# Optimization experiments

Measured on AMD Instinct MI355X. Metric: run time of the kernel, lower is better.

## Reference

```python
import jax, jax.numpy as jnp
import numpy as np

ALPHA = 0.2  # LeakyReLU negative slope
NUM_HEADS, OUT_DIM = 8, 16
N_NODES, N_EDGES, IN_DIM = 50000, 800000, 128


def setup_inputs() -> dict:
    key = jax.random.key(0)
    k = jax.random.split(key, 6)
    return {
        "x": jax.random.normal(k[0], (N_NODES, IN_DIM), dtype=jnp.float32),
        "W1": jax.random.normal(k[1], (IN_DIM, IN_DIM), dtype=jnp.float32) * (1.414 / np.sqrt(IN_DIM)),
        "W2": jax.random.normal(k[2], (NUM_HEADS * OUT_DIM, IN_DIM), dtype=jnp.float32) * (1.414 / np.sqrt(IN_DIM)),
        "attn_l": jax.random.normal(k[3], (NUM_HEADS, OUT_DIM), dtype=jnp.float32) * 0.3,
        "attn_r": jax.random.normal(k[4], (NUM_HEADS, OUT_DIM), dtype=jnp.float32) * 0.3,
        "edge_index": jax.random.randint(k[5], (2, N_EDGES), 0, N_NODES, dtype=jnp.int64),
    }


def reference(x, W1, W2, attn_l, attn_r, edge_index):
    N = x.shape[0]
    H, D = attn_l.shape
    # fc1 -> leaky_relu -> fc2, reshape to per-head features [N, H, D]
    h2 = jax.nn.leaky_relu(x @ W1.T, ALPHA)
    ft = (h2 @ W2.T).reshape(N, H, D)
    # per-node attention halves: a1 = ft . attn_l, a2 = ft . attn_r  -> [N, H]
    a1 = jnp.einsum('nhd,hd->nh', ft, attn_l)
    a2 = jnp.einsum('nhd,hd->nh', ft, attn_r)
    src, dst = edge_index[0], edge_index[1]
    # edge attention logits [E, H]
    e = jax.nn.leaky_relu(a1[src] + a2[dst], ALPHA)
    # edge softmax normalized over incoming edges of each dst node
    emax = jax.ops.segment_max(e, dst, num_segments=N)
    ee = jnp.exp(e - emax[dst])
    esum = jax.ops.segment_sum(ee, dst, num_segments=N)
    a = ee / esum[dst]  # [E, H]
    # weighted scatter-sum aggregation: sum_{e: dst(e)=n} a_e * ft[src(e)]
    msg = ft[src] * a[:, :, None]  # [E, H, D]
    out = jax.ops.segment_sum(msg, dst, num_segments=N)  # [N, H, D]
    return out
```

## Files before the change

### kernel.cpp

```cpp
#include <hip/hip_runtime.h>

#define ALPHA 0.2f
constexpr int N = 50000;
constexpr int E = 800000;

typedef __attribute__((ext_vector_type(8))) short bf16x8;
typedef __attribute__((ext_vector_type(4))) float f32x4;

__device__ inline ushort f2bf(float v) {
  uint u = __float_as_uint(v);
  return (ushort)((u + 0x7fff + ((u >> 16) & 1)) >> 16);
}
__device__ inline float bf2f(ushort u) { return __uint_as_float(((uint)u) << 16); }

constexpr int LDX = 136;

constexpr int BN   = 128;
constexpr int NB   = (N + BN - 1) / BN;
constexpr int NBP  = 512;
constexpr int PSTR = 392;
constexpr int CHUNK = 4096;
constexpr int NBLK  = (E + CHUNK - 1) / CHUNK;
constexpr int FROWS = 32;
constexpr int FEATB = (N + FROWS - 1) / FROWS;
constexpr int SMEMB = 2 * FROWS * LDX * 2;

__global__ __launch_bounds__(256) void k1_kernel(const float* __restrict__ W1,
    const float* __restrict__ W2, ushort* __restrict__ wf1hi, ushort* __restrict__ wf1lo,
    ushort* __restrict__ wf2hi, ushort* __restrict__ wf2lo,
    const int* __restrict__ dst, int* __restrict__ partial) {
  const int bid = blockIdx.x;
  const int t = threadIdx.x;
  if (bid < NBLK) {
    __shared__ int lh[NB];
    const int e0 = bid * CHUNK, e1 = min(e0 + CHUNK, E);
    for (int i = t; i < NB; i += 256) lh[i] = 0;
    __syncthreads();
    for (int i = e0 + t; i < e1; i += 256)
      atomicAdd(&lh[((unsigned)dst[i]) >> 7], 1);
    __syncthreads();
    for (int i = t; i < NB; i += 256) partial[bid * PSTR + i] = lh[i];
    return;
  }
  int g = (bid - NBLK) * 256 + t;
  const float* W = (g < 2048) ? W1 : W2;
  ushort* whi = (g < 2048) ? wf1hi : wf2hi;
  ushort* wlo = (g < 2048) ? wf1lo : wf2lo;
  int f = g & 2047;
  int ks = f >> 9, rem = f & 511, jb = rem >> 6, l = rem & 63;
  int m = jb * 16 + (l & 15), kb = ks * 32 + (l >> 4) * 8;
#pragma unroll
  for (int q = 0; q < 2; ++q) {
    float4 v = *(const float4*)&W[m * 128 + kb + q * 4];
    ushort4 hi, lo;
    hi.x = f2bf(v.x); lo.x = f2bf(v.x - bf2f(hi.x));
    hi.y = f2bf(v.y); lo.y = f2bf(v.y - bf2f(hi.y));
    hi.z = f2bf(v.z); lo.z = f2bf(v.z - bf2f(hi.z));
    hi.w = f2bf(v.w); lo.w = f2bf(v.w - bf2f(hi.w));
    *(ushort4*)&whi[f * 8 + q * 4] = hi;
    *(ushort4*)&wlo[f * 8 + q * 4] = lo;
  }
}

__global__ __launch_bounds__(NBP) void colscan_kernel(const int* __restrict__ partial,
    int* __restrict__ bucket_base, int* __restrict__ chunk_base) {
  __shared__ int sh[NBP];
  const int t = threadIdx.x;
  int tot = 0;
  if (t < NB)
    for (int blk = 0; blk < NBLK; ++blk) tot += partial[blk * PSTR + t];
  sh[t] = (t < NB) ? tot : 0;
  __syncthreads();
  for (int off = 1; off < NBP; off <<= 1) {
    int u = (t >= off) ? sh[t - off] : 0;
    __syncthreads();
    sh[t] += u;
    __syncthreads();
  }
  if (t < NB) {
    int base = sh[t] - tot;
    bucket_base[t] = base;
    int run = base;
    for (int blk = 0; blk < NBLK; ++blk) {
      chunk_base[blk * PSTR + t] = run;
      run += partial[blk * PSTR + t];
    }
  }
  if (t == NB - 1) bucket_base[NB] = sh[t];
}

__global__ __launch_bounds__(256, 6) void featpart_kernel(
    const float* __restrict__ x,
    const ushort* __restrict__ wf1hi, const ushort* __restrict__ wf1lo,
    const ushort* __restrict__ wf2hi, const ushort* __restrict__ wf2lo,
    const float* __restrict__ attn_l, const float* __restrict__ attn_r,
    ushort* __restrict__ ft_bf, float* __restrict__ a1, float* __restrict__ a2,
    const int* __restrict__ src, const int* __restrict__ dst,
    const int* __restrict__ chunk_base, int* __restrict__ ebuf) {
  extern __shared__ char smem[];
  const int bid = blockIdx.x;
  const int tid = threadIdx.x;

  if (bid < NBLK) {
    int* curs = (int*)smem;
    const int e0 = bid * CHUNK, e1 = min(e0 + CHUNK, E);
    for (int k = tid; k < NB; k += 256) curs[k] = chunk_base[bid * PSTR + k];
    __syncthreads();
    for (int i = e0 + tid; i < e1; i += 256) {
      int s = src[i], d = dst[i];
      int pos = atomicAdd(&curs[((unsigned)d) >> 7], 1);
      ebuf[pos] = (s << 7) | (d & 127);
    }
    return;
  }

  ushort* sXhi = (ushort*)smem;
  ushort* sXlo = sXhi + FROWS * LDX;
  const int w = tid >> 6, l = tid & 63;
  const int lr = l & 15, lg4 = l >> 4;
  const int rowBase = (bid - NBLK) * FROWS;

  for (int i = tid; i < FROWS * 32; i += 256) {
    int row = i >> 5, kc = i & 31;
    int g = rowBase + row;
    float4 v = make_float4(0.f, 0.f, 0.f, 0.f);
    if (g < N) v = reinterpret_cast<const float4*>(x)[g * 32 + kc];
    ushort4 hi, lo;
    hi.x = f2bf(v.x); lo.x = f2bf(v.x - bf2f(hi.x));
    hi.y = f2bf(v.y); lo.y = f2bf(v.y - bf2f(hi.y));
    hi.z = f2bf(v.z); lo.z = f2bf(v.z - bf2f(hi.z));
    hi.w = f2bf(v.w); lo.w = f2bf(v.w - bf2f(hi.w));
    *(ushort4*)&sXhi[row * LDX + kc * 4] = hi;
    *(ushort4*)&sXlo[row * LDX + kc * 4] = lo;
  }
  __syncthreads();

  f32x4 acc[2][2];
#pragma unroll
  for (int mi = 0; mi < 2; ++mi)
#pragma unroll
    for (int jj = 0; jj < 2; ++jj) acc[mi][jj] = (f32x4){0.f, 0.f, 0.f, 0.f};

#pragma unroll
  for (int ks = 0; ks < 4; ++ks) {
    bf16x8 bh[2], bl[2], ah[2], al[2];
#pragma unroll
    for (int jj = 0; jj < 2; ++jj) {
      int off = ((ks * 8 + (2 * w + jj)) * 64 + l) * 8;
      bh[jj] = *(const bf16x8*)&wf1hi[off];
      bl[jj] = *(const bf16x8*)&wf1lo[off];
    }
#pragma unroll
    for (int mi = 0; mi < 2; ++mi) {
      int addr = (mi * 16 + lr) * LDX + ks * 32 + lg4 * 8;
      ah[mi] = *(const bf16x8*)&sXhi[addr];
      al[mi] = *(const bf16x8*)&sXlo[addr];
    }
#pragma unroll
    for (int mi = 0; mi < 2; ++mi)
#pragma unroll
      for (int jj = 0; jj < 2; ++jj) {
        acc[mi][jj] = __builtin_amdgcn_mfma_f32_16x16x32_bf16(ah[mi], bh[jj], acc[mi][jj], 0, 0, 0);
        acc[mi][jj] = __builtin_amdgcn_mfma_f32_16x16x32_bf16(ah[mi], bl[jj], acc[mi][jj], 0, 0, 0);
        acc[mi][jj] = __builtin_amdgcn_mfma_f32_16x16x32_bf16(al[mi], bh[jj], acc[mi][jj], 0, 0, 0);
      }
  }
  __syncthreads();

#pragma unroll
  for (int mi = 0; mi < 2; ++mi)
#pragma unroll
    for (int jj = 0; jj < 2; ++jj)
#pragma unroll
      for (int r = 0; r < 4; ++r) {
        float v = acc[mi][jj][r];
        v = v > 0.f ? v : ALPHA * v;
        int row = mi * 16 + lg4 * 4 + r;
        int col = w * 32 + jj * 16 + lr;
        ushort hv = f2bf(v);
        sXhi[row * LDX + col] = hv;
        sXlo[row * LDX + col] = f2bf(v - bf2f(hv));
      }
  __syncthreads();

#pragma unroll
  for (int mi = 0; mi < 2; ++mi)
#pragma unroll
    for (int jj = 0; jj < 2; ++jj) acc[mi][jj] = (f32x4){0.f, 0.f, 0.f, 0.f};

#pragma unroll
  for (int ks = 0; ks < 4; ++ks) {
    bf16x8 bh[2], bl[2], ah[2], al[2];
#pragma unroll
    for (int jj = 0; jj < 2; ++jj) {
      int off = ((ks * 8 + (2 * w + jj)) * 64 + l) * 8;
      bh[jj] = *(const bf16x8*)&wf2hi[off];
      bl[jj] = *(const bf16x8*)&wf2lo[off];
    }
#pragma unroll
    for (int mi = 0; mi < 2; ++mi) {
      int addr = (mi * 16 + lr) * LDX + ks * 32 + lg4 * 8;
      ah[mi] = *(const bf16x8*)&sXhi[addr];
      al[mi] = *(const bf16x8*)&sXlo[addr];
    }
#pragma unroll
    for (int mi = 0; mi < 2; ++mi)
#pragma unroll
      for (int jj = 0; jj < 2; ++jj) {
        acc[mi][jj] = __builtin_amdgcn_mfma_f32_16x16x32_bf16(ah[mi], bh[jj], acc[mi][jj], 0, 0, 0);
        acc[mi][jj] = __builtin_amdgcn_mfma_f32_16x16x32_bf16(ah[mi], bl[jj], acc[mi][jj], 0, 0, 0);
        acc[mi][jj] = __builtin_amdgcn_mfma_f32_16x16x32_bf16(al[mi], bh[jj], acc[mi][jj], 0, 0, 0);
      }
  }

#pragma unroll
  for (int mi = 0; mi < 2; ++mi)
#pragma unroll
    for (int jj = 0; jj < 2; ++jj) {
      int h = 2 * w + jj;
      float alv = attn_l[h * 16 + lr], arv = attn_r[h * 16 + lr];
#pragma unroll
      for (int r = 0; r < 4; ++r) {
        float v = acc[mi][jj][r];
        int grow = rowBase + mi * 16 + lg4 * 4 + r;
        bool valid = grow < N;
        if (valid) ft_bf[grow * 128 + h * 16 + lr] = f2bf(v);
        float sl = v * alv, sr = v * arv;
#pragma unroll
        for (int off = 8; off; off >>= 1) {
          sl += __shfl_xor(sl, off, 16);
          sr += __shfl_xor(sr, off, 16);
        }
        if (valid && lr == 0) { a1[grow * 8 + h] = sl; a2[grow * 8 + h] = sr; }
      }
    }
}

__global__ __launch_bounds__(256) void fine_kernel(const int* __restrict__ ebuf,
    const int* __restrict__ bucket_base, int* __restrict__ row_ptr,
    int* __restrict__ col_src) {
  __shared__ int ldeg[BN], sc[BN], curs[BN];
  const int b = blockIdx.x, t = threadIdx.x;
  const int node0 = b * BN;
  const int nloc = min(BN, N - node0);
  const int bstart = bucket_base[b], bend = bucket_base[b + 1];
  if (t < BN) ldeg[t] = 0;
  __syncthreads();
  for (int i = bstart + t; i < bend; i += 256)
    atomicAdd(&ldeg[ebuf[i] & 127], 1);
  __syncthreads();
  if (t < BN) sc[t] = ldeg[t];
  __syncthreads();
#pragma unroll
  for (int off = 1; off < BN; off <<= 1) {
    int u = (t < BN && t >= off) ? sc[t - off] : 0;
    __syncthreads();
    if (t < BN) sc[t] += u;
    __syncthreads();
  }
  if (t < nloc) {
    int base = bstart + sc[t] - ldeg[t];
    row_ptr[node0 + t] = base;
    curs[t] = base;
  }
  if (b == NB - 1 && t == 0) row_ptr[N] = bend;
  __syncthreads();
  for (int i = bstart + t; i < bend; i += 256) {
    int pr = ebuf[i];
    int pos = atomicAdd(&curs[pr & 127], 1);
    col_src[pos] = pr >> 7;
  }
}

__global__ __launch_bounds__(256) void agg_kernel(const int* __restrict__ row_ptr,
    const int* __restrict__ col_src, const ushort* __restrict__ ft_bf,
    const float* __restrict__ a1, const float* __restrict__ a2,
    float* __restrict__ out) {
  const int node = blockIdx.x * 4 + (threadIdx.x >> 6);
  if (node >= N) return;
  const int t = threadIdx.x & 63;
  const int eSlot = t >> 3;
  const int hA = t & 7;
  const int hB = t >> 3;
  const int start = row_ptr[node], end = row_ptr[node + 1];
  const float a2nA = a2[node * 8 + hA];

  float l = 0.f, acc0 = 0.f, acc1 = 0.f;
  for (int base = start; base < end; base += 8) {
    int rem = end - base; rem = rem > 8 ? 8 : rem;
    int idx = base + (eSlot < rem ? eSlot : rem - 1);
    int s = col_src[idx];
    float lg = a1[s * 8 + hA] + a2nA;
    lg = lg > 0.f ? lg : ALPHA * lg;
    float p = (eSlot < rem) ? __expf(lg) : 0.f;
#pragma unroll
    for (int e = 0; e < 8; ++e) {
      float pe = __shfl(p, e * 8 + hB);
      int se = __shfl(s, e * 8);
      ushort2 f = *(const ushort2*)&ft_bf[se * 128 + t * 2];
      l += pe;
      acc0 = fmaf(pe, bf2f(f.x), acc0);
      acc1 = fmaf(pe, bf2f(f.y), acc1);
    }
  }
  float inv = (end > start) ? 1.f / l : 0.f;
  *(float2*)&out[node * 128 + t * 2] = make_float2(acc0 * inv, acc1 * inv);
}

extern "C" void kernel_launch(void* const* d_in, const int* in_sizes, int n_in,
                              void* d_out, int out_size, void* d_ws, size_t ws_size,
                              hipStream_t stream) {
  const float* x      = (const float*)d_in[0];
  const float* W1     = (const float*)d_in[1];
  const float* W2     = (const float*)d_in[2];
  const float* attn_l = (const float*)d_in[3];
  const float* attn_r = (const float*)d_in[4];
  const int*   edge   = (const int*)d_in[5];
  const int*   src    = edge;
  const int*   dst    = edge + E;
  float* out = (float*)d_out;

  char* ws = (char*)d_ws;
  ushort* ft_bf       = (ushort*)(ws);
  float*  a1          = (float*) (ws + 12800000);
  float*  a2          = (float*) (ws + 14400000);
  int*    row_ptr     = (int*)   (ws + 16000000);
  int*    bucket_base = (int*)   (ws + 16200064);
  int*    col_src     = (int*)   (ws + 16201664);
  ushort* wf1hi       = (ushort*)(ws + 19401664);
  ushort* wf1lo       = (ushort*)(ws + 19434432);
  ushort* wf2hi       = (ushort*)(ws + 19467200);
  ushort* wf2lo       = (ushort*)(ws + 19499968);
  int*    ebuf        = (int*)   (ws + 19532736);
  int*    partial     = (int*)   (ws + 22732736);
  int*    chunk_base  = (int*)   (ws + 23040064);

  k1_kernel<<<NBLK + 16, 256, 0, stream>>>(W1, W2, wf1hi, wf1lo, wf2hi, wf2lo, dst, partial);
  colscan_kernel<<<1, NBP, 0, stream>>>(partial, bucket_base, chunk_base);
  featpart_kernel<<<NBLK + FEATB, 256, SMEMB, stream>>>(
      x, wf1hi, wf1lo, wf2hi, wf2lo, attn_l, attn_r, ft_bf, a1, a2,
      src, dst, chunk_base, ebuf);
  fine_kernel<<<NB, 256, 0, stream>>>(ebuf, bucket_base, row_ptr, col_src);
  agg_kernel<<<(N + 3) / 4, 256, 0, stream>>>(row_ptr, col_src, ft_bf, a1, a2, out);
}
```

Baseline: 98.37 us.

## Fuse fine CSR build into aggregation kernel using shared-memory edge lists

Merges the fine bucket-sort kernel and the aggregation kernel. Each block handles a 32-node quarter of a 128-node bucket, builds its local CSR in shared memory, then aggregates directly from it. This removes one launch and the global row_ptr/col_src round trip. In exchange, each of the four blocks per bucket rescans the whole bucket's ebuf, and only 4 waves handle 32 nodes serially, which lowers parallelism per node. The local edge buffer is capped at 1024 entries, so a larger quarter would silently drop edges. Unroll pragmas are also added to the colscan loops.

```diff
diff --git a/kernel.cpp b/kernel.cpp
--- a/kernel.cpp
+++ b/kernel.cpp
@@ -24,6 +24,7 @@
 constexpr int FROWS = 32;
 constexpr int FEATB = (N + FROWS - 1) / FROWS;
 constexpr int SMEMB = 2 * FROWS * LDX * 2;
+constexpr int QCAP  = 1024;
 
 __global__ __launch_bounds__(256) void k1_kernel(const float* __restrict__ W1,
     const float* __restrict__ W2, ushort* __restrict__ wf1hi, ushort* __restrict__ wf1lo,
@@ -67,8 +68,10 @@
   __shared__ int sh[NBP];
   const int t = threadIdx.x;
   int tot = 0;
-  if (t < NB)
+  if (t < NB) {
+#pragma unroll 4
     for (int blk = 0; blk < NBLK; ++blk) tot += partial[blk * PSTR + t];
+  }
   sh[t] = (t < NB) ? tot : 0;
   __syncthreads();
   for (int off = 1; off < NBP; off <<= 1) {
@@ -81,6 +84,7 @@
     int base = sh[t] - tot;
     bucket_base[t] = base;
     int run = base;
+#pragma unroll 4
     for (int blk = 0; blk < NBLK; ++blk) {
       chunk_base[blk * PSTR + t] = run;
       run += partial[blk * PSTR + t];
@@ -236,75 +240,76 @@
     }
 }
 
-__global__ __launch_bounds__(256) void fine_kernel(const int* __restrict__ ebuf,
-    const int* __restrict__ bucket_base, int* __restrict__ row_ptr,
-    int* __restrict__ col_src) {
-  __shared__ int ldeg[BN], sc[BN], curs[BN];
-  const int b = blockIdx.x, t = threadIdx.x;
-  const int node0 = b * BN;
-  const int nloc = min(BN, N - node0);
+__global__ __launch_bounds__(256) void fineagg_kernel(const int* __restrict__ ebuf,
+    const int* __restrict__ bucket_base, const ushort* __restrict__ ft_bf,
+    const float* __restrict__ a1, const float* __restrict__ a2,
+    float* __restrict__ out) {
+  __shared__ int ldeg[32], lbase[32], curs[32];
+  __shared__ int lbuf[QCAP];
+  const int bid = blockIdx.x;
+  const int b = bid >> 2, qq = bid & 3;
+  const int t = threadIdx.x;
   const int bstart = bucket_base[b], bend = bucket_base[b + 1];
-  if (t < BN) ldeg[t] = 0;
-  __syncthreads();
-  for (int i = bstart + t; i < bend; i += 256)
-    atomicAdd(&ldeg[ebuf[i] & 127], 1);
-  __syncthreads();
-  if (t < BN) sc[t] = ldeg[t];
-  __syncthreads();
-#pragma unroll
-  for (int off = 1; off < BN; off <<= 1) {
-    int u = (t < BN && t >= off) ? sc[t - off] : 0;
-    __syncthreads();
-    if (t < BN) sc[t] += u;
-    __syncthreads();
-  }
-  if (t < nloc) {
-    int base = bstart + sc[t] - ldeg[t];
-    row_ptr[node0 + t] = base;
-    curs[t] = base;
-  }
-  if (b == NB - 1 && t == 0) row_ptr[N] = bend;
+
+  if (t < 32) ldeg[t] = 0;
+  __syncthreads();
+  for (int i = bstart + t; i < bend; i += 256) {
+    int dl = ebuf[i] & 127;
+    if ((dl >> 5) == qq) atomicAdd(&ldeg[dl & 31], 1);
+  }
+  __syncthreads();
+  int v = (t < 32) ? ldeg[t] : 0;
+  int sc = v;
+#pragma unroll
+  for (int off = 1; off < 32; off <<= 1) {
+    int u = __shfl_up(sc, off, 64);
+    if ((t & 63) >= off) sc += u;
+  }
+  if (t < 32) { lbase[t] = sc - v; curs[t] = sc - v; }
   __syncthreads();
   for (int i = bstart + t; i < bend; i += 256) {
     int pr = ebuf[i];
-    int pos = atomicAdd(&curs[pr & 127], 1);
-    col_src[pos] = pr >> 7;
-  }
-}
-
-__global__ __launch_bounds__(256) void agg_kernel(const int* __restrict__ row_ptr,
-    const int* __restrict__ col_src, const ushort* __restrict__ ft_bf,
-    const float* __restrict__ a1, const float* __restrict__ a2,
-    float* __restrict__ out) {
-  const int node = blockIdx.x * 4 + (threadIdx.x >> 6);
-  if (node >= N) return;
-  const int t = threadIdx.x & 63;
-  const int eSlot = t >> 3;
-  const int hA = t & 7;
-  const int hB = t >> 3;
-  const int start = row_ptr[node], end = row_ptr[node + 1];
-  const float a2nA = a2[node * 8 + hA];
-
-  float l = 0.f, acc0 = 0.f, acc1 = 0.f;
-  for (int base = start; base < end; base += 8) {
-    int rem = end - base; rem = rem > 8 ? 8 : rem;
-    int idx = base + (eSlot < rem ? eSlot : rem - 1);
-    int s = col_src[idx];
-    float lg = a1[s * 8 + hA] + a2nA;
-    lg = lg > 0.f ? lg : ALPHA * lg;
-    float p = (eSlot < rem) ? __expf(lg) : 0.f;
-#pragma unroll
-    for (int e = 0; e < 8; ++e) {
-      float pe = __shfl(p, e * 8 + hB);
-      int se = __shfl(s, e * 8);
-      ushort2 f = *(const ushort2*)&ft_bf[se * 128 + t * 2];
-      l += pe;
-      acc0 = fmaf(pe, bf2f(f.x), acc0);
-      acc1 = fmaf(pe, bf2f(f.y), acc1);
-    }
-  }
-  float inv = (end > start) ? 1.f / l : 0.f;
-  *(float2*)&out[node * 128 + t * 2] = make_float2(acc0 * inv, acc1 * inv);
+    int dl = pr & 127;
+    if ((dl >> 5) == qq) {
+      int pos = atomicAdd(&curs[dl & 31], 1);
+      if (pos < QCAP) lbuf[pos] = pr >> 7;
+    }
+  }
+  __syncthreads();
+
+  const int g = t >> 6;
+  const int tl = t & 63;
+  const int eSlot = tl >> 3;
+  const int hA = tl & 7;
+  const int hB = tl >> 3;
+  for (int j = 0; j < 8; ++j) {
+    int loc = qq * 32 + g * 8 + j;
+    int node = b * BN + loc;
+    if (node >= N) continue;
+    int lloc = loc & 31;
+    int start = lbase[lloc], end = start + ldeg[lloc];
+    const float a2nA = a2[node * 8 + hA];
+    float l = 0.f, acc0 = 0.f, acc1 = 0.f;
+    for (int base = start; base < end; base += 8) {
+      int rem = end - base; rem = rem > 8 ? 8 : rem;
+      int idx = base + (eSlot < rem ? eSlot : rem - 1);
+      int s = lbuf[idx];
+      float lg = a1[s * 8 + hA] + a2nA;
+      lg = lg > 0.f ? lg : ALPHA * lg;
+      float p = (eSlot < rem) ? __expf(lg) : 0.f;
+#pragma unroll
+      for (int e = 0; e < 8; ++e) {
+        float pe = __shfl(p, e * 8 + hB);
+        int se = __shfl(s, e * 8);
+        ushort2 f = *(const ushort2*)&ft_bf[se * 128 + tl * 2];
+        l += pe;
+        acc0 = fmaf(pe, bf2f(f.x), acc0);
+        acc1 = fmaf(pe, bf2f(f.y), acc1);
+      }
+    }
+    float inv = (end > start) ? 1.f / l : 0.f;
+    *(float2*)&out[node * 128 + tl * 2] = make_float2(acc0 * inv, acc1 * inv);
+  }
 }
 
 extern "C" void kernel_launch(void* const* d_in, const int* in_sizes, int n_in,
@@ -324,22 +329,19 @@
   ushort* ft_bf       = (ushort*)(ws);
   float*  a1          = (float*) (ws + 12800000);
   float*  a2          = (float*) (ws + 14400000);
-  int*    row_ptr     = (int*)   (ws + 16000000);
-  int*    bucket_base = (int*)   (ws + 16200064);
-  int*    col_src     = (int*)   (ws + 16201664);
-  ushort* wf1hi       = (ushort*)(ws + 19401664);
-  ushort* wf1lo       = (ushort*)(ws + 19434432);
-  ushort* wf2hi       = (ushort*)(ws + 19467200);
-  ushort* wf2lo       = (ushort*)(ws + 19499968);
-  int*    ebuf        = (int*)   (ws + 19532736);
-  int*    partial     = (int*)   (ws + 22732736);
-  int*    chunk_base  = (int*)   (ws + 23040064);
+  int*    bucket_base = (int*)   (ws + 16000000);
+  ushort* wf1hi       = (ushort*)(ws + 16001600);
+  ushort* wf1lo       = (ushort*)(ws + 16034368);
+  ushort* wf2hi       = (ushort*)(ws + 16067136);
+  ushort* wf2lo       = (ushort*)(ws + 16099904);
+  int*    ebuf        = (int*)   (ws + 16132672);
+  int*    partial     = (int*)   (ws + 19332672);
+  int*    chunk_base  = (int*)   (ws + 19640000);
 
   k1_kernel<<<NBLK + 16, 256, 0, stream>>>(W1, W2, wf1hi, wf1lo, wf2hi, wf2lo, dst, partial);
   colscan_kernel<<<1, NBP, 0, stream>>>(partial, bucket_base, chunk_base);
   featpart_kernel<<<NBLK + FEATB, 256, SMEMB, stream>>>(
       x, wf1hi, wf1lo, wf2hi, wf2lo, attn_l, attn_r, ft_bf, a1, a2,
       src, dst, chunk_base, ebuf);
-  fine_kernel<<<NB, 256, 0, stream>>>(ebuf, bucket_base, row_ptr, col_src);
-  agg_kernel<<<(N + 3) / 4, 256, 0, stream>>>(row_ptr, col_src, ft_bf, a1, a2, out);
-}
+  fineagg_kernel<<<NB * 4, 256, 0, stream>>>(ebuf, bucket_base, ft_bf, a1, a2, out);
+}
```

After: 107.0 us. 1.09x slower.

## Sort each node's CSR edges into coarse source-id bins and enlarge edge chunks

Applied to the files above, without the earlier changes.

The fine CSR-build kernel now keys edges by (destination node, source-id bin of 8192 nodes), so that within each destination row the source indices are roughly grouped by region. The intent is better locality for the ft_bf gathers in the aggregation kernel. The edge chunk size for the coarse histogram is doubled, which halves the partial-histogram rows the single-block colscan must walk, and those scan loops get an unroll hint. In exchange, the fine kernel runs a larger 1024-entry shared-memory scan with more barriers.

```diff
diff --git a/kernel.cpp b/kernel.cpp
--- a/kernel.cpp
+++ b/kernel.cpp
@@ -19,11 +19,13 @@
 constexpr int NB   = (N + BN - 1) / BN;
 constexpr int NBP  = 512;
 constexpr int PSTR = 392;
-constexpr int CHUNK = 4096;
+constexpr int CHUNK = 8192;
 constexpr int NBLK  = (E + CHUNK - 1) / CHUNK;
 constexpr int FROWS = 32;
 constexpr int FEATB = (N + FROWS - 1) / FROWS;
 constexpr int SMEMB = 2 * FROWS * LDX * 2;
+constexpr int NBIN  = 8;
+constexpr int NKEY  = BN * NBIN;
 
 __global__ __launch_bounds__(256) void k1_kernel(const float* __restrict__ W1,
     const float* __restrict__ W2, ushort* __restrict__ wf1hi, ushort* __restrict__ wf1lo,
@@ -67,8 +69,10 @@
   __shared__ int sh[NBP];
   const int t = threadIdx.x;
   int tot = 0;
-  if (t < NB)
+  if (t < NB) {
+#pragma unroll 4
     for (int blk = 0; blk < NBLK; ++blk) tot += partial[blk * PSTR + t];
+  }
   sh[t] = (t < NB) ? tot : 0;
   __syncthreads();
   for (int off = 1; off < NBP; off <<= 1) {
@@ -81,6 +85,7 @@
     int base = sh[t] - tot;
     bucket_base[t] = base;
     int run = base;
+#pragma unroll 4
     for (int blk = 0; blk < NBLK; ++blk) {
       chunk_base[blk * PSTR + t] = run;
       run += partial[blk * PSTR + t];
@@ -239,35 +244,36 @@
 __global__ __launch_bounds__(256) void fine_kernel(const int* __restrict__ ebuf,
     const int* __restrict__ bucket_base, int* __restrict__ row_ptr,
     int* __restrict__ col_src) {
-  __shared__ int ldeg[BN], sc[BN], curs[BN];
+  __shared__ int ldeg[NKEY], sA[NKEY], sB[NKEY], curs[NKEY];
   const int b = blockIdx.x, t = threadIdx.x;
   const int node0 = b * BN;
   const int nloc = min(BN, N - node0);
   const int bstart = bucket_base[b], bend = bucket_base[b + 1];
-  if (t < BN) ldeg[t] = 0;
-  __syncthreads();
-  for (int i = bstart + t; i < bend; i += 256)
-    atomicAdd(&ldeg[ebuf[i] & 127], 1);
-  __syncthreads();
-  if (t < BN) sc[t] = ldeg[t];
-  __syncthreads();
-#pragma unroll
-  for (int off = 1; off < BN; off <<= 1) {
-    int u = (t < BN && t >= off) ? sc[t - off] : 0;
-    __syncthreads();
-    if (t < BN) sc[t] += u;
-    __syncthreads();
-  }
-  if (t < nloc) {
-    int base = bstart + sc[t] - ldeg[t];
-    row_ptr[node0 + t] = base;
-    curs[t] = base;
-  }
-  if (b == NB - 1 && t == 0) row_ptr[N] = bend;
+  for (int k = t; k < NKEY; k += 256) ldeg[k] = 0;
   __syncthreads();
   for (int i = bstart + t; i < bend; i += 256) {
     int pr = ebuf[i];
-    int pos = atomicAdd(&curs[pr & 127], 1);
+    int key = ((pr & 127) << 3) | ((pr >> 7) >> 13);
+    atomicAdd(&ldeg[key], 1);
+  }
+  __syncthreads();
+  for (int k = t; k < NKEY; k += 256) sA[k] = ldeg[k];
+  __syncthreads();
+  int* pin = sA; int* pout = sB;
+  for (int off = 1; off < NKEY; off <<= 1) {
+    for (int k = t; k < NKEY; k += 256)
+      pout[k] = pin[k] + ((k >= off) ? pin[k - off] : 0);
+    __syncthreads();
+    int* tmp = pin; pin = pout; pout = tmp;
+  }
+  for (int k = t; k < NKEY; k += 256) curs[k] = bstart + pin[k] - ldeg[k];
+  __syncthreads();
+  if (t < nloc) row_ptr[node0 + t] = curs[t * NBIN];
+  if (b == NB - 1 && t == 0) row_ptr[N] = bend;
+  for (int i = bstart + t; i < bend; i += 256) {
+    int pr = ebuf[i];
+    int key = ((pr & 127) << 3) | ((pr >> 7) >> 13);
+    int pos = atomicAdd(&curs[key], 1);
     col_src[pos] = pr >> 7;
   }
 }
@@ -333,7 +339,7 @@
   ushort* wf2lo       = (ushort*)(ws + 19499968);
   int*    ebuf        = (int*)   (ws + 19532736);
   int*    partial     = (int*)   (ws + 22732736);
-  int*    chunk_base  = (int*)   (ws + 23040064);
+  int*    chunk_base  = (int*)   (ws + 22886400);
 
   k1_kernel<<<NBLK + 16, 256, 0, stream>>>(W1, W2, wf1hi, wf1lo, wf2hi, wf2lo, dst, partial);
   colscan_kernel<<<1, NBP, 0, stream>>>(partial, bucket_base, chunk_base);
```

Measured after the change: 111.0 us. +12.8%, slower.

## Parallelize bucket prefix scan across blocks with transposed partial counts

Applied to the files above, without the earlier changes.

Replaces the single-block column scan, which serially walked all chunk partials per bucket twice, with a two-stage scan. Partial histograms are stored transposed so that one block per bucket scans across chunks in parallel, and a small second kernel scans the bucket totals. The partition kernel then adds the bucket base to the chunk-relative offset. The cost is one extra kernel launch and strided writes in the histogram kernel.

```diff
diff --git a/kernel.cpp b/kernel.cpp
--- a/kernel.cpp
+++ b/kernel.cpp
@@ -18,9 +18,9 @@
 constexpr int BN   = 128;
 constexpr int NB   = (N + BN - 1) / BN;
 constexpr int NBP  = 512;
-constexpr int PSTR = 392;
 constexpr int CHUNK = 4096;
 constexpr int NBLK  = (E + CHUNK - 1) / CHUNK;
+constexpr int CSTR  = 200;
 constexpr int FROWS = 32;
 constexpr int FEATB = (N + FROWS - 1) / FROWS;
 constexpr int SMEMB = 2 * FROWS * LDX * 2;
@@ -28,7 +28,7 @@
 __global__ __launch_bounds__(256) void k1_kernel(const float* __restrict__ W1,
     const float* __restrict__ W2, ushort* __restrict__ wf1hi, ushort* __restrict__ wf1lo,
     ushort* __restrict__ wf2hi, ushort* __restrict__ wf2lo,
-    const int* __restrict__ dst, int* __restrict__ partial) {
+    const int* __restrict__ dst, int* __restrict__ partialT) {
   const int bid = blockIdx.x;
   const int t = threadIdx.x;
   if (bid < NBLK) {
@@ -39,7 +39,7 @@
     for (int i = e0 + t; i < e1; i += 256)
       atomicAdd(&lh[((unsigned)dst[i]) >> 7], 1);
     __syncthreads();
-    for (int i = t; i < NB; i += 256) partial[bid * PSTR + i] = lh[i];
+    for (int i = t; i < NB; i += 256) partialT[i * CSTR + bid] = lh[i];
     return;
   }
   int g = (bid - NBLK) * 256 + t;
@@ -62,14 +62,29 @@
   }
 }
 
-__global__ __launch_bounds__(NBP) void colscan_kernel(const int* __restrict__ partial,
-    int* __restrict__ bucket_base, int* __restrict__ chunk_base) {
+__global__ __launch_bounds__(256) void colscanA_kernel(const int* __restrict__ partialT,
+    int* __restrict__ chunkrel, int* __restrict__ btot) {
+  __shared__ int sh[256];
+  const int b = blockIdx.x, t = threadIdx.x;
+  int v = (t < NBLK) ? partialT[b * CSTR + t] : 0;
+  sh[t] = v;
+  __syncthreads();
+  for (int off = 1; off < 256; off <<= 1) {
+    int u = (t >= off) ? sh[t - off] : 0;
+    __syncthreads();
+    sh[t] += u;
+    __syncthreads();
+  }
+  if (t < NBLK) chunkrel[b * CSTR + t] = sh[t] - v;
+  if (t == 255) btot[b] = sh[255];
+}
+
+__global__ __launch_bounds__(NBP) void colscanB_kernel(const int* __restrict__ btot,
+    int* __restrict__ bucket_base) {
   __shared__ int sh[NBP];
   const int t = threadIdx.x;
-  int tot = 0;
-  if (t < NB)
-    for (int blk = 0; blk < NBLK; ++blk) tot += partial[blk * PSTR + t];
-  sh[t] = (t < NB) ? tot : 0;
+  int v = (t < NB) ? btot[t] : 0;
+  sh[t] = v;
   __syncthreads();
   for (int off = 1; off < NBP; off <<= 1) {
     int u = (t >= off) ? sh[t - off] : 0;
@@ -77,15 +92,7 @@
     sh[t] += u;
     __syncthreads();
   }
-  if (t < NB) {
-    int base = sh[t] - tot;
-    bucket_base[t] = base;
-    int run = base;
-    for (int blk = 0; blk < NBLK; ++blk) {
-      chunk_base[blk * PSTR + t] = run;
-      run += partial[blk * PSTR + t];
-    }
-  }
+  if (t < NB) bucket_base[t] = sh[t] - v;
   if (t == NB - 1) bucket_base[NB] = sh[t];
 }
 
@@ -96,7 +103,8 @@
     const float* __restrict__ attn_l, const float* __restrict__ attn_r,
     ushort* __restrict__ ft_bf, float* __restrict__ a1, float* __restrict__ a2,
     const int* __restrict__ src, const int* __restrict__ dst,
-    const int* __restrict__ chunk_base, int* __restrict__ ebuf) {
+    const int* __restrict__ bucket_base, const int* __restrict__ chunkrel,
+    int* __restrict__ ebuf) {
   extern __shared__ char smem[];
   const int bid = blockIdx.x;
   const int tid = threadIdx.x;
@@ -104,7 +112,8 @@
   if (bid < NBLK) {
     int* curs = (int*)smem;
     const int e0 = bid * CHUNK, e1 = min(e0 + CHUNK, E);
-    for (int k = tid; k < NB; k += 256) curs[k] = chunk_base[bid * PSTR + k];
+    for (int k = tid; k < NB; k += 256)
+      curs[k] = bucket_base[k] + chunkrel[k * CSTR + bid];
     __syncthreads();
     for (int i = e0 + tid; i < e1; i += 256) {
       int s = src[i], d = dst[i];
@@ -332,14 +341,16 @@
   ushort* wf2hi       = (ushort*)(ws + 19467200);
   ushort* wf2lo       = (ushort*)(ws + 19499968);
   int*    ebuf        = (int*)   (ws + 19532736);
-  int*    partial     = (int*)   (ws + 22732736);
-  int*    chunk_base  = (int*)   (ws + 23040064);
-
-  k1_kernel<<<NBLK + 16, 256, 0, stream>>>(W1, W2, wf1hi, wf1lo, wf2hi, wf2lo, dst, partial);
-  colscan_kernel<<<1, NBP, 0, stream>>>(partial, bucket_base, chunk_base);
+  int*    partialT    = (int*)   (ws + 22732736);
+  int*    chunkrel    = (int*)   (ws + 23045536);
+  int*    btot        = (int*)   (ws + 23358336);
+
+  k1_kernel<<<NBLK + 16, 256, 0, stream>>>(W1, W2, wf1hi, wf1lo, wf2hi, wf2lo, dst, partialT);
+  colscanA_kernel<<<NB, 256, 0, stream>>>(partialT, chunkrel, btot);
+  colscanB_kernel<<<1, NBP, 0, stream>>>(btot, bucket_base);
   featpart_kernel<<<NBLK + FEATB, 256, SMEMB, stream>>>(
       x, wf1hi, wf1lo, wf2hi, wf2lo, attn_l, attn_r, ft_bf, a1, a2,
-      src, dst, chunk_base, ebuf);
+      src, dst, bucket_base, chunkrel, ebuf);
   fine_kernel<<<NB, 256, 0, stream>>>(ebuf, bucket_base, row_ptr, col_src);
   agg_kernel<<<(N + 3) / 4, 256, 0, stream>>>(row_ptr, col_src, ft_bf, a1, a2, out);
 }
```

Result: faster. 90.25 us (median of 2 runs) (-8.3%).
